# Optimization experiments

Measured on AMD Instinct MI355X. Metric: run time of the kernel, lower is better.

Reference implementation:

```python
import jax, jax.numpy as jnp
import numpy as np

N = 50000
E = 800000
IN_C = 128
HID = 64
HEADS = 4
NEG_SLOPE = 0.2
EPS = 1e-16


def setup_inputs() -> dict:
    key = jax.random.key(0)
    ks = jax.random.split(key, 12)
    x = jax.random.normal(ks[0], (N, IN_C), dtype=jnp.float32)
    edge_index = jax.random.randint(ks[1], (2, E), 0, N, dtype=jnp.int64)
    # layer 1: in -> (HEADS, HID), concat heads
    W1 = jax.random.normal(ks[2], (IN_C, HEADS * HID), dtype=jnp.float32) * (1.0 / np.sqrt(IN_C))
    a_src1 = jax.random.normal(ks[3], (HEADS, HID), dtype=jnp.float32) * 0.1
    a_dst1 = jax.random.normal(ks[4], (HEADS, HID), dtype=jnp.float32) * 0.1
    b1 = jnp.zeros((HEADS * HID,), dtype=jnp.float32)
    # layer 2: HEADS*HID -> (1, HID)
    W2 = jax.random.normal(ks[5], (HEADS * HID, HID), dtype=jnp.float32) * (1.0 / np.sqrt(HEADS * HID))
    a_src2 = jax.random.normal(ks[6], (1, HID), dtype=jnp.float32) * 0.1
    a_dst2 = jax.random.normal(ks[7], (1, HID), dtype=jnp.float32) * 0.1
    b2 = jnp.zeros((HID,), dtype=jnp.float32)
    return {"x": x, "edge_index": edge_index, "W1": W1, "a_src1": a_src1,
            "a_dst1": a_dst1, "b1": b1, "W2": W2, "a_src2": a_src2,
            "a_dst2": a_dst2, "b2": b2}


def _gat_conv(x, src, dst, W, a_src, a_dst, bias, heads, ch):
    n = x.shape[0]
    h = (x @ W).reshape(n, heads, ch)                       # [N,H,C]
    alpha_s = jnp.einsum('nhc,hc->nh', h, a_src)            # [N,H]
    alpha_d = jnp.einsum('nhc,hc->nh', h, a_dst)            # [N,H]
    e = jax.nn.leaky_relu(alpha_s[src] + alpha_d[dst], NEG_SLOPE)  # [E,H]
    # segment softmax over incoming edges of each dst node
    m = jax.ops.segment_max(e, dst, num_segments=n)         # [N,H]
    ex = jnp.exp(e - m[dst])
    denom = jax.ops.segment_sum(ex, dst, num_segments=n)    # [N,H]
    alpha = ex / (denom[dst] + EPS)                         # [E,H]
    msg = h[src] * alpha[:, :, None]                        # [E,H,C]
    out = jax.ops.segment_sum(msg, dst, num_segments=n)     # [N,H,C]
    return out.reshape(n, heads * ch) + bias


def reference(x, edge_index, W1, a_src1, a_dst1, b1, W2, a_src2, a_dst2, b2):
    src = edge_index[0]
    dst = edge_index[1]
    h = _gat_conv(x, src, dst, W1, a_src1, a_dst1, b1, HEADS, HID)
    h = jax.nn.elu(h)
    h = _gat_conv(h, src, dst, W2, a_src2, a_dst2, b2, 1, HID)
    h = jax.nn.elu(h)
    return h  # [N, HID] (output_dim == hidden_channels so no final linear)
```

## Files before the change

kernel.cpp:

```cpp
#include <hip/hip_runtime.h>
#include <math.h>

#define NN 50000
#define EE 800000
#define IN_C 128
#define HID 64
#define HEADS 4
#define SCAN_BLOCKS ((NN + 255) / 256)
#define EBLOCKS ((EE + 255) / 256)

typedef __attribute__((ext_vector_type(8))) short bf16x8;
typedef __attribute__((ext_vector_type(4))) float f32x4;

#if defined(__has_builtin)
#if __has_builtin(__builtin_amdgcn_fdot2_f32_bf16)
#define HAVE_FDOT2_BF16 1
#endif
#endif


__device__ inline unsigned short f2bf(float f) {
    unsigned u = __float_as_uint(f);
    return (unsigned short)((u + 0x7fff + ((u >> 16) & 1)) >> 16);
}
__device__ inline float bf2f(unsigned short s) {
    return __uint_as_float(((unsigned)s) << 16);
}
__device__ inline unsigned prm(unsigned a, unsigned b, unsigned sel) {
    return __builtin_amdgcn_perm(a, b, sel);
}
#ifdef HAVE_FDOT2_BF16
typedef __attribute__((ext_vector_type(2))) __bf16 bf2v;
__device__ inline float fdot2bf(unsigned h, unsigned w, float acc) {
    return __builtin_amdgcn_fdot2_f32_bf16(__builtin_bit_cast(bf2v, h),
                                           __builtin_bit_cast(bf2v, w), acc, false);
}
#else
__device__ inline float fdot2bf(unsigned h, unsigned w, float acc) {
    return acc + bf2f((unsigned short)(h & 0xffff)) * bf2f((unsigned short)(w & 0xffff))
               + bf2f((unsigned short)(h >> 16)) * bf2f((unsigned short)(w >> 16));
}
#endif

__device__ inline int wave_incl_scan(int v, int lane) {
    #pragma unroll
    for (int off = 1; off < 64; off <<= 1) {
        int t = __shfl_up(v, off);
        if (lane >= off) v += t;
    }
    return v;
}

__device__ inline int block256_excl_scan(int v, int tid, int* ws4) {
    int lane = tid & 63, wv = tid >> 6;
    int incl = wave_incl_scan(v, lane);
    if (lane == 63) ws4[wv] = incl;
    __syncthreads();
    if (tid == 0) {
        int run = 0;
        #pragma unroll
        for (int i = 0; i < 4; i++) { int t = ws4[i]; ws4[i] = run; run += t; }
    }
    __syncthreads();
    return incl + ws4[wv] - v;
}


__global__ void front_kernel(const int* __restrict__ ei, int* __restrict__ deg,
                             unsigned short* __restrict__ rank,
                             const float* __restrict__ W1, unsigned short* __restrict__ W1Thi,
                             unsigned short* __restrict__ W1Tlo,
                             const float* __restrict__ W2, unsigned short* __restrict__ W2Thi,
                             unsigned short* __restrict__ W2Tlo) {
    int b = blockIdx.x;
    int tid = threadIdx.x;
    if (b < EBLOCKS) {
        int i = b * 256 + tid;
        if (i < EE) rank[i] = (unsigned short)atomicAdd(&deg[ei[EE + i]], 1);
    } else if (b < EBLOCKS + 128) {
        int idx = (b - EBLOCKS) * 256 + tid;
        int r = idx >> 8, c = idx & 255;
        float v = W1[idx];
        unsigned short h = f2bf(v);
        W1Thi[c * 128 + r] = h;
        W1Tlo[c * 128 + r] = f2bf(v - bf2f(h));
    } else {
        int idx = (b - EBLOCKS - 128) * 256 + tid;
        int r = idx >> 6, c = idx & 63;
        float v = W2[idx];
        unsigned short h = f2bf(v);
        W2Thi[c * 256 + r] = h;
        W2Tlo[c * 256 + r] = f2bf(v - bf2f(h));
    }
}

__global__ void scan_fill_kernel(const int* __restrict__ deg,
                                 unsigned long long* __restrict__ desc,
                                 int* __restrict__ row_ptr) {
    __shared__ int ws4[4];
    __shared__ int sbase;
    int b = blockIdx.x, tid = threadIdx.x;
    int idx = b * 256 + tid;
    int d = (idx < NN) ? deg[idx] : 0;
    int excl = block256_excl_scan(d, tid, ws4);
    if (tid == 255) {
        unsigned total = (unsigned)(excl + d);
        __threadfence();
        atomicExch(&desc[b], (1ULL << 32) | (unsigned long long)total);
    }
    if (tid < 64) {
        int sum = 0;
        int hi = b;
        while (hi > 0) {
            int lo = hi - 64; if (lo < 0) lo = 0;
            int myi = lo + tid;
            unsigned v = 0;
            if (myi < hi) {
                unsigned long long d8;
                do { d8 = atomicAdd(&desc[myi], 0ULL); } while ((d8 >> 32) == 0);
                v = (unsigned)(d8 & 0xffffffffULL);
            }
            #pragma unroll
            for (int off = 32; off; off >>= 1) v += __shfl_down(v, off);
            v = __shfl(v, 0);
            sum += (int)v;
            hi = lo;
        }
        if (tid == 0) sbase = sum;
    }
    __syncthreads();
    int gbase = sbase;
    if (idx < NN) row_ptr[idx] = gbase + excl;
    if (b == gridDim.x - 1 && tid == 255) row_ptr[NN] = gbase + excl + d;
}

__global__ void scatter_kernel(const int* __restrict__ ei, const unsigned short* __restrict__ rank,
                               const int* __restrict__ row_ptr, unsigned short* __restrict__ csr_src) {
    int i = blockIdx.x * blockDim.x + threadIdx.x;
    if (i < EE) {
        int d = ei[EE + i];
        csr_src[row_ptr[d] + (int)rank[i]] = (unsigned short)ei[i];
    }
}

__global__ __launch_bounds__(256) void gemm1_mfma(
        const float* __restrict__ x,
        const unsigned short* __restrict__ Bhi, const unsigned short* __restrict__ Blo,
        const float* __restrict__ a_src, const float* __restrict__ a_dst,
        unsigned short* __restrict__ h1b, float* __restrict__ as1, float* __restrict__ ad1) {
    __shared__ unsigned short Ahi[64][136];
    __shared__ unsigned short Alo[64][136];
    int tid = threadIdx.x;
    int w = tid >> 6, lane = tid & 63;
    int lq = lane >> 4, lr = lane & 15;
    int brow = blockIdx.x * 64;
    {
        int row = tid >> 2;
        int col0 = (tid & 3) * 32;
        int gr = min(brow + row, NN - 1);
        #pragma unroll
        for (int i = 0; i < 32; i += 4) {
            float4 v = *(const float4*)(x + (size_t)gr * 128 + col0 + i);
            unsigned short h0 = f2bf(v.x), h1 = f2bf(v.y), h2 = f2bf(v.z), h3 = f2bf(v.w);
            Ahi[row][col0 + i + 0] = h0; Alo[row][col0 + i + 0] = f2bf(v.x - bf2f(h0));
            Ahi[row][col0 + i + 1] = h1; Alo[row][col0 + i + 1] = f2bf(v.y - bf2f(h1));
            Ahi[row][col0 + i + 2] = h2; Alo[row][col0 + i + 2] = f2bf(v.z - bf2f(h2));
            Ahi[row][col0 + i + 3] = h3; Alo[row][col0 + i + 3] = f2bf(v.w - bf2f(h3));
        }
    }
    __syncthreads();
    f32x4 acc[4][4];
    f32x4 zf = {0.f, 0.f, 0.f, 0.f};
    #pragma unroll
    for (int mi = 0; mi < 4; mi++)
        #pragma unroll
        for (int ni = 0; ni < 4; ni++) acc[mi][ni] = zf;
    #pragma unroll
    for (int q = 0; q < 4; q++) {
        int ko = q * 32 + lq * 8;
        bf16x8 ah[4], al[4];
        #pragma unroll
        for (int mi = 0; mi < 4; mi++) {
            ah[mi] = *(const bf16x8*)(const void*)&Ahi[mi * 16 + lr][ko];
            al[mi] = *(const bf16x8*)(const void*)&Alo[mi * 16 + lr][ko];
        }
        #pragma unroll
        for (int ni = 0; ni < 4; ni++) {
            size_t bo = (size_t)(w * 64 + ni * 16 + lr) * 128 + ko;
            bf16x8 bh = *(const bf16x8*)(const void*)(Bhi + bo);
            bf16x8 bl = *(const bf16x8*)(const void*)(Blo + bo);
            #pragma unroll
            for (int mi = 0; mi < 4; mi++) {
                acc[mi][ni] = __builtin_amdgcn_mfma_f32_16x16x32_bf16(al[mi], bh, acc[mi][ni], 0, 0, 0);
                acc[mi][ni] = __builtin_amdgcn_mfma_f32_16x16x32_bf16(ah[mi], bl, acc[mi][ni], 0, 0, 0);
                acc[mi][ni] = __builtin_amdgcn_mfma_f32_16x16x32_bf16(ah[mi], bh, acc[mi][ni], 0, 0, 0);
            }
        }
    }
    float asv[4], adv[4];
    #pragma unroll
    for (int ni = 0; ni < 4; ni++) {
        asv[ni] = a_src[w * 64 + ni * 16 + lr];
        adv[ni] = a_dst[w * 64 + ni * 16 + lr];
    }
    #pragma unroll
    for (int mi = 0; mi < 4; mi++) {
        f32x4 ps = zf, pd = zf;
        #pragma unroll
        for (int ni = 0; ni < 4; ni++)
            #pragma unroll
            for (int r = 0; r < 4; r++) {
                ps[r] += acc[mi][ni][r] * asv[ni];
                pd[r] += acc[mi][ni][r] * adv[ni];
            }
        #pragma unroll
        for (int m = 1; m < 16; m <<= 1)
            #pragma unroll
            for (int r = 0; r < 4; r++) {
                ps[r] += __shfl_xor(ps[r], m);
                pd[r] += __shfl_xor(pd[r], m);
            }
        #pragma unroll
        for (int r = 0; r < 4; r++) {
            int n = brow + mi * 16 + lq * 4 + r;
            if (lr == 0 && n < NN) { as1[n * 4 + w] = ps[r]; ad1[n * 4 + w] = pd[r]; }
        }
        #pragma unroll
        for (int ni = 0; ni < 4; ni++)
            #pragma unroll
            for (int r = 0; r < 4; r++) {
                int n = brow + mi * 16 + lq * 4 + r;
                if (n < NN)
                    h1b[(size_t)n * 256 + w * 64 + ni * 16 + lr] = f2bf(acc[mi][ni][r]);
            }
    }
}

__global__ __launch_bounds__(256) void gemm2_mfma(
        const unsigned short* __restrict__ Ab,
        const unsigned short* __restrict__ Bhi, const unsigned short* __restrict__ Blo,
        const float* __restrict__ a_src, const float* __restrict__ a_dst,
        unsigned short* __restrict__ g2b, float* __restrict__ as2, float* __restrict__ ad2) {
    int tid = threadIdx.x;
    int w = tid >> 6, lane = tid & 63;
    int lq = lane >> 4, lr = lane & 15;
    int wrow = blockIdx.x * 128 + w * 32;
    f32x4 acc[2][4];
    f32x4 zf = {0.f, 0.f, 0.f, 0.f};
    #pragma unroll
    for (int mi = 0; mi < 2; mi++)
        #pragma unroll
        for (int ni = 0; ni < 4; ni++) acc[mi][ni] = zf;
    int ra = min(wrow + lr, NN - 1);
    int rb = min(wrow + 16 + lr, NN - 1);
    #pragma unroll
    for (int q = 0; q < 8; q++) {
        int ko = q * 32 + lq * 8;
        bf16x8 ah0 = *(const bf16x8*)(const void*)(Ab + (size_t)ra * 256 + ko);
        bf16x8 ah1 = *(const bf16x8*)(const void*)(Ab + (size_t)rb * 256 + ko);
        #pragma unroll
        for (int ni = 0; ni < 4; ni++) {
            size_t bo = (size_t)(ni * 16 + lr) * 256 + ko;
            bf16x8 bh = *(const bf16x8*)(const void*)(Bhi + bo);
            bf16x8 bl = *(const bf16x8*)(const void*)(Blo + bo);
            acc[0][ni] = __builtin_amdgcn_mfma_f32_16x16x32_bf16(ah0, bl, acc[0][ni], 0, 0, 0);
            acc[0][ni] = __builtin_amdgcn_mfma_f32_16x16x32_bf16(ah0, bh, acc[0][ni], 0, 0, 0);
            acc[1][ni] = __builtin_amdgcn_mfma_f32_16x16x32_bf16(ah1, bl, acc[1][ni], 0, 0, 0);
            acc[1][ni] = __builtin_amdgcn_mfma_f32_16x16x32_bf16(ah1, bh, acc[1][ni], 0, 0, 0);
        }
    }
    float asv[4], adv[4];
    #pragma unroll
    for (int ni = 0; ni < 4; ni++) {
        asv[ni] = a_src[ni * 16 + lr];
        adv[ni] = a_dst[ni * 16 + lr];
    }
    #pragma unroll
    for (int mi = 0; mi < 2; mi++) {
        f32x4 ps = zf, pd = zf;
        #pragma unroll
        for (int ni = 0; ni < 4; ni++)
            #pragma unroll
            for (int r = 0; r < 4; r++) {
                ps[r] += acc[mi][ni][r] * asv[ni];
                pd[r] += acc[mi][ni][r] * adv[ni];
            }
        #pragma unroll
        for (int m = 1; m < 16; m <<= 1)
            #pragma unroll
            for (int r = 0; r < 4; r++) {
                ps[r] += __shfl_xor(ps[r], m);
                pd[r] += __shfl_xor(pd[r], m);
            }
        #pragma unroll
        for (int r = 0; r < 4; r++) {
            int n = wrow + mi * 16 + lq * 4 + r;
            if (lr == 0 && n < NN) { as2[n] = ps[r]; ad2[n] = pd[r]; }
        }
        #pragma unroll
        for (int ni = 0; ni < 4; ni++)
            #pragma unroll
            for (int r = 0; r < 4; r++) {
                int n = wrow + mi * 16 + lq * 4 + r;
                if (n < NN)
                    g2b[(size_t)n * 64 + ni * 16 + lr] = f2bf(acc[mi][ni][r]);
            }
    }
}

__global__ __launch_bounds__(256) void agg1_kernel(
        const unsigned short* __restrict__ h1b, const int* __restrict__ row_ptr,
        const unsigned short* __restrict__ csr_src, const float* __restrict__ as,
        const float* __restrict__ ad, const float* __restrict__ b1,
        unsigned short* __restrict__ h2b) {
    __shared__ int            ssrc[4][64];
    __shared__ unsigned short wbf[4][4][64];
    int tid = threadIdx.x;
    int wv = tid >> 6, lane = tid & 63;
    int n = blockIdx.x * 4 + wv;
    if (n >= NN) return;
    int start = row_ptr[n], end = row_ptr[n + 1];
    float4 adv = ((const float4*)ad)[n];
    int whead = lane >> 4;
    float4 acc = make_float4(0.f, 0.f, 0.f, 0.f);
    float d0 = 0.f, d1 = 0.f, d2 = 0.f, d3 = 0.f;
    for (int c0 = start; c0 < end; c0 += 64) {
        int m = min(64, end - c0);
        if (lane < m) {
            int s = (int)csr_src[c0 + lane];
            ssrc[wv][lane] = s;
            float4 asv = ((const float4*)as)[s];
            float e0 = asv.x + adv.x; e0 = e0 > 0.f ? e0 : 0.2f * e0; float x0 = __expf(e0);
            float e1 = asv.y + adv.y; e1 = e1 > 0.f ? e1 : 0.2f * e1; float x1 = __expf(e1);
            float e2 = asv.z + adv.z; e2 = e2 > 0.f ? e2 : 0.2f * e2; float x2 = __expf(e2);
            float e3 = asv.w + adv.w; e3 = e3 > 0.f ? e3 : 0.2f * e3; float x3 = __expf(e3);
            wbf[wv][0][lane] = f2bf(x0);
            wbf[wv][1][lane] = f2bf(x1);
            wbf[wv][2][lane] = f2bf(x2);
            wbf[wv][3][lane] = f2bf(x3);
            d0 += x0; d1 += x1; d2 += x2; d3 += x3;
        }
        int j = 0;
        for (; j + 8 <= m; j += 8) {
            int sj[8]; uint2 hj[8];
            #pragma unroll
            for (int u = 0; u < 8; u++) sj[u] = ssrc[wv][j + u];
            #pragma unroll
            for (int u = 0; u < 8; u++)
                hj[u] = ((const uint2*)h1b)[(size_t)sj[u] * 64 + lane];
            unsigned wp01 = *(const unsigned*)&wbf[wv][whead][j];
            unsigned wp23 = *(const unsigned*)&wbf[wv][whead][j + 2];
            unsigned wp45 = *(const unsigned*)&wbf[wv][whead][j + 4];
            unsigned wp67 = *(const unsigned*)&wbf[wv][whead][j + 6];
            acc.x = fdot2bf(prm(hj[1].x, hj[0].x, 0x05040100), wp01, acc.x);
            acc.y = fdot2bf(prm(hj[1].x, hj[0].x, 0x07060302), wp01, acc.y);
            acc.z = fdot2bf(prm(hj[1].y, hj[0].y, 0x05040100), wp01, acc.z);
            acc.w = fdot2bf(prm(hj[1].y, hj[0].y, 0x07060302), wp01, acc.w);
            acc.x = fdot2bf(prm(hj[3].x, hj[2].x, 0x05040100), wp23, acc.x);
            acc.y = fdot2bf(prm(hj[3].x, hj[2].x, 0x07060302), wp23, acc.y);
            acc.z = fdot2bf(prm(hj[3].y, hj[2].y, 0x05040100), wp23, acc.z);
            acc.w = fdot2bf(prm(hj[3].y, hj[2].y, 0x07060302), wp23, acc.w);
            acc.x = fdot2bf(prm(hj[5].x, hj[4].x, 0x05040100), wp45, acc.x);
            acc.y = fdot2bf(prm(hj[5].x, hj[4].x, 0x07060302), wp45, acc.y);
            acc.z = fdot2bf(prm(hj[5].y, hj[4].y, 0x05040100), wp45, acc.z);
            acc.w = fdot2bf(prm(hj[5].y, hj[4].y, 0x07060302), wp45, acc.w);
            acc.x = fdot2bf(prm(hj[7].x, hj[6].x, 0x05040100), wp67, acc.x);
            acc.y = fdot2bf(prm(hj[7].x, hj[6].x, 0x07060302), wp67, acc.y);
            acc.z = fdot2bf(prm(hj[7].y, hj[6].y, 0x05040100), wp67, acc.z);
            acc.w = fdot2bf(prm(hj[7].y, hj[6].y, 0x07060302), wp67, acc.w);
        }
        for (; j + 2 <= m; j += 2) {
            int s0 = ssrc[wv][j], s1 = ssrc[wv][j + 1];
            uint2 ha = ((const uint2*)h1b)[(size_t)s0 * 64 + lane];
            uint2 hb = ((const uint2*)h1b)[(size_t)s1 * 64 + lane];
            unsigned wp = *(const unsigned*)&wbf[wv][whead][j];
            acc.x = fdot2bf(prm(hb.x, ha.x, 0x05040100), wp, acc.x);
            acc.y = fdot2bf(prm(hb.x, ha.x, 0x07060302), wp, acc.y);
            acc.z = fdot2bf(prm(hb.y, ha.y, 0x05040100), wp, acc.z);
            acc.w = fdot2bf(prm(hb.y, ha.y, 0x07060302), wp, acc.w);
        }
        if (j < m) {
            int s = ssrc[wv][j];
            float w = bf2f(wbf[wv][whead][j]);
            ushort4 hv = ((const ushort4*)h1b)[(size_t)s * 64 + lane];
            acc.x += bf2f(hv.x) * w; acc.y += bf2f(hv.y) * w;
            acc.z += bf2f(hv.z) * w; acc.w += bf2f(hv.w) * w;
        }
    }
    #pragma unroll
    for (int off = 32; off; off >>= 1) {
        d0 += __shfl_down(d0, off); d1 += __shfl_down(d1, off);
        d2 += __shfl_down(d2, off); d3 += __shfl_down(d3, off);
    }
    d0 = __shfl(d0, 0); d1 = __shfl(d1, 0);
    d2 = __shfl(d2, 0); d3 = __shfl(d3, 0);
    float den = whead == 0 ? d0 : whead == 1 ? d1 : whead == 2 ? d2 : d3;
    float inv = 1.f / (den + 1e-16f);
    float4 bv = ((const float4*)b1)[lane];
    float4 r;
    r.x = acc.x * inv + bv.x; r.y = acc.y * inv + bv.y;
    r.z = acc.z * inv + bv.z; r.w = acc.w * inv + bv.w;
    r.x = r.x > 0.f ? r.x : expm1f(r.x);
    r.y = r.y > 0.f ? r.y : expm1f(r.y);
    r.z = r.z > 0.f ? r.z : expm1f(r.z);
    r.w = r.w > 0.f ? r.w : expm1f(r.w);
    ushort4 hv;
    hv.x = f2bf(r.x); hv.y = f2bf(r.y); hv.z = f2bf(r.z); hv.w = f2bf(r.w);
    ((ushort4*)h2b)[(size_t)n * 64 + lane] = hv;
}

__global__ __launch_bounds__(256) void agg2_kernel(
        const unsigned short* __restrict__ g2b, const int* __restrict__ row_ptr,
        const unsigned short* __restrict__ csr_src, const float* __restrict__ as,
        const float* __restrict__ ad, const float* __restrict__ b2,
        float* __restrict__ out) {
    __shared__ int            ssrc[4][64];
    __shared__ unsigned short wbf[4][64];
    int tid = threadIdx.x;
    int wv = tid >> 6, lane = tid & 63;
    int n = blockIdx.x * 4 + wv;
    if (n >= NN) return;
    int start = row_ptr[n], end = row_ptr[n + 1];
    float adv = ad[n];
    float acc = 0.f;
    float den = 0.f;
    for (int c0 = start; c0 < end; c0 += 64) {
        int m = min(64, end - c0);
        if (lane < m) {
            int s = (int)csr_src[c0 + lane];
            ssrc[wv][lane] = s;
            float e = as[s] + adv;
            e = e > 0.f ? e : 0.2f * e;
            float x = __expf(e);
            wbf[wv][lane] = f2bf(x);
            den += x;
        }
        int j = 0;
        for (; j + 8 <= m; j += 8) {
            int sj[8]; unsigned gj[8];
            #pragma unroll
            for (int u = 0; u < 8; u++) sj[u] = ssrc[wv][j + u];
            #pragma unroll
            for (int u = 0; u < 8; u++)
                gj[u] = g2b[(size_t)sj[u] * 64 + lane];
            unsigned wp01 = *(const unsigned*)&wbf[wv][j];
            unsigned wp23 = *(const unsigned*)&wbf[wv][j + 2];
            unsigned wp45 = *(const unsigned*)&wbf[wv][j + 4];
            unsigned wp67 = *(const unsigned*)&wbf[wv][j + 6];
            acc = fdot2bf(prm(gj[1], gj[0], 0x05040100), wp01, acc);
            acc = fdot2bf(prm(gj[3], gj[2], 0x05040100), wp23, acc);
            acc = fdot2bf(prm(gj[5], gj[4], 0x05040100), wp45, acc);
            acc = fdot2bf(prm(gj[7], gj[6], 0x05040100), wp67, acc);
        }
        for (; j + 2 <= m; j += 2) {
            int s0 = ssrc[wv][j], s1 = ssrc[wv][j + 1];
            unsigned g0 = g2b[(size_t)s0 * 64 + lane];
            unsigned g1 = g2b[(size_t)s1 * 64 + lane];
            unsigned wp = *(const unsigned*)&wbf[wv][j];
            acc = fdot2bf(prm(g1, g0, 0x05040100), wp, acc);
        }
        if (j < m) {
            int s = ssrc[wv][j];
            acc += bf2f(g2b[(size_t)s * 64 + lane]) * bf2f(wbf[wv][j]);
        }
    }
    #pragma unroll
    for (int off = 32; off; off >>= 1) den += __shfl_down(den, off);
    den = __shfl(den, 0);
    float inv = 1.f / (den + 1e-16f);
    float r = acc * inv + b2[lane];
    out[(size_t)n * 64 + lane] = r > 0.f ? r : expm1f(r);
}


extern "C" void kernel_launch(void* const* d_in, const int* in_sizes, int n_in,
                              void* d_out, int out_size, void* d_ws, size_t ws_size,
                              hipStream_t stream) {
    const float* x      = (const float*)d_in[0];
    const int*   ei     = (const int*)d_in[1];
    const float* W1     = (const float*)d_in[2];
    const float* a_src1 = (const float*)d_in[3];
    const float* a_dst1 = (const float*)d_in[4];
    const float* b1     = (const float*)d_in[5];
    const float* W2     = (const float*)d_in[6];
    const float* a_src2 = (const float*)d_in[7];
    const float* a_dst2 = (const float*)d_in[8];
    const float* b2     = (const float*)d_in[9];
    float* out = (float*)d_out;

    char* base = (char*)d_ws;
    size_t off = 0;
    auto alloc = [&](size_t bytes) -> void* {
        void* p = base + off;
        off = (off + bytes + 255) & ~(size_t)255;
        return p;
    };
    int*   deg     = (int*)alloc(NN * sizeof(int));
    unsigned long long* desc = (unsigned long long*)alloc(SCAN_BLOCKS * sizeof(unsigned long long));
    unsigned short* rank = (unsigned short*)alloc(EE * sizeof(unsigned short));
    int*   row_ptr = (int*)alloc((NN + 1) * sizeof(int));
    unsigned short* csr_src = (unsigned short*)alloc(EE * sizeof(unsigned short));
    unsigned short* W1Thi = (unsigned short*)alloc(256 * 128 * 2);
    unsigned short* W1Tlo = (unsigned short*)alloc(256 * 128 * 2);
    unsigned short* W2Thi = (unsigned short*)alloc(64 * 256 * 2);
    unsigned short* W2Tlo = (unsigned short*)alloc(64 * 256 * 2);
    unsigned short* h1b   = (unsigned short*)alloc((size_t)NN * 256 * 2);
    float* as1     = (float*)alloc((size_t)NN * 4 * sizeof(float));
    float* ad1     = (float*)alloc((size_t)NN * 4 * sizeof(float));
    unsigned short* h2b   = (unsigned short*)alloc((size_t)NN * 256 * 2);
    unsigned short* g2b   = (unsigned short*)alloc((size_t)NN * 64 * 2);
    float* as2     = (float*)alloc((size_t)NN * sizeof(float));
    float* ad2     = (float*)alloc((size_t)NN * sizeof(float));

    size_t clear_bytes = (size_t)((char*)(desc + SCAN_BLOCKS) - (char*)deg);
    hipMemsetAsync(deg, 0, clear_bytes, stream);

    front_kernel<<<EBLOCKS + 128 + 64, 256, 0, stream>>>(ei, deg, rank, W1, W1Thi, W1Tlo,
                                                         W2, W2Thi, W2Tlo);
    scan_fill_kernel<<<SCAN_BLOCKS, 256, 0, stream>>>(deg, desc, row_ptr);
    scatter_kernel<<<EBLOCKS, 256, 0, stream>>>(ei, rank, row_ptr, csr_src);

    gemm1_mfma<<<(NN + 63) / 64, 256, 0, stream>>>(x, W1Thi, W1Tlo,
                                                   a_src1, a_dst1, h1b, as1, ad1);
    agg1_kernel<<<(NN + 3) / 4, 256, 0, stream>>>(h1b, row_ptr, csr_src, as1, ad1, b1, h2b);
    gemm2_mfma<<<(NN + 127) / 128, 256, 0, stream>>>(h2b, W2Thi, W2Tlo,
                                                     a_src2, a_dst2, g2b, as2, ad2);
    agg2_kernel<<<(NN + 3) / 4, 256, 0, stream>>>(g2b, row_ptr, csr_src, as2, ad2, b2, out);
}
```

Baseline: 281.4 us.

## Precompute edge softmax weights in CSR order and pad rows to four

Edge attention weights (exp of leaky-relu logits) and per-node denominators are now computed once per edge in a scatter pass, which writes bf16 weights in CSR order and accumulates denominators with atomics. The separate scatter kernel is folded into that pass. Rows are padded to multiples of four with zero entries, so the aggregation kernels drop their remainder loops and process two edges per half-wave with a software-pipelined double-buffered gather of wider vectors. This moves exp work out of the latency-bound gather loops, at the cost of float atomics, extra memory traffic for the weight arrays, and an extra kernel per layer.

```diff
diff --git a/kernel.cpp b/kernel.cpp
--- a/kernel.cpp
+++ b/kernel.cpp
@@ -6,6 +6,7 @@
 #define IN_C 128
 #define HID 64
 #define HEADS 4
+#define EEP 950000
 #define SCAN_BLOCKS ((NN + 255) / 256)
 #define EBLOCKS ((EE + 255) / 256)
 
@@ -96,12 +97,16 @@
 
 __global__ void scan_fill_kernel(const int* __restrict__ deg,
                                  unsigned long long* __restrict__ desc,
-                                 int* __restrict__ row_ptr) {
+                                 int* __restrict__ row_ptr,
+                                 unsigned short* __restrict__ csr_src,
+                                 unsigned short* __restrict__ w1t,
+                                 unsigned short* __restrict__ w2t) {
     __shared__ int ws4[4];
     __shared__ int sbase;
     int b = blockIdx.x, tid = threadIdx.x;
     int idx = b * 256 + tid;
-    int d = (idx < NN) ? deg[idx] : 0;
+    int draw = (idx < NN) ? deg[idx] : 0;
+    int d = (draw + 3) & ~3;
     int excl = block256_excl_scan(d, tid, ws4);
     if (tid == 255) {
         unsigned total = (unsigned)(excl + d);
@@ -130,17 +135,16 @@
     }
     __syncthreads();
     int gbase = sbase;
-    if (idx < NN) row_ptr[idx] = gbase + excl;
+    if (idx < NN) {
+        int rp = gbase + excl;
+        row_ptr[idx] = rp;
+        for (int p = rp + draw; p < rp + d; ++p) {
+            csr_src[p] = 0;
+            w2t[p] = 0;
+            w1t[p] = 0; w1t[EEP + p] = 0; w1t[2 * EEP + p] = 0; w1t[3 * EEP + p] = 0;
+        }
+    }
     if (b == gridDim.x - 1 && tid == 255) row_ptr[NN] = gbase + excl + d;
-}
-
-__global__ void scatter_kernel(const int* __restrict__ ei, const unsigned short* __restrict__ rank,
-                               const int* __restrict__ row_ptr, unsigned short* __restrict__ csr_src) {
-    int i = blockIdx.x * blockDim.x + threadIdx.x;
-    if (i < EE) {
-        int d = ei[EE + i];
-        csr_src[row_ptr[d] + (int)rank[i]] = (unsigned short)ei[i];
-    }
 }
 
 __global__ __launch_bounds__(256) void gemm1_mfma(
@@ -308,168 +312,179 @@
     }
 }
 
-__global__ __launch_bounds__(256) void agg1_kernel(
+__global__ __launch_bounds__(256) void scatter_w1_kernel(
+        const int* __restrict__ ei, const unsigned short* __restrict__ rank,
+        const int* __restrict__ row_ptr, const float* __restrict__ as1,
+        const float* __restrict__ ad1, unsigned short* __restrict__ csr_src,
+        unsigned short* __restrict__ w1t, float* __restrict__ den1) {
+    int i = blockIdx.x * 256 + threadIdx.x;
+    if (i >= EE) return;
+    int s = ei[i], d = ei[EE + i];
+    int pos = row_ptr[d] + (int)rank[i];
+    csr_src[pos] = (unsigned short)s;
+    float4 av = ((const float4*)as1)[s];
+    float4 bv = ((const float4*)ad1)[d];
+    float e0 = av.x + bv.x; e0 = e0 > 0.f ? e0 : 0.2f * e0; float x0 = __expf(e0);
+    float e1 = av.y + bv.y; e1 = e1 > 0.f ? e1 : 0.2f * e1; float x1 = __expf(e1);
+    float e2 = av.z + bv.z; e2 = e2 > 0.f ? e2 : 0.2f * e2; float x2 = __expf(e2);
+    float e3 = av.w + bv.w; e3 = e3 > 0.f ? e3 : 0.2f * e3; float x3 = __expf(e3);
+    w1t[pos]           = f2bf(x0);
+    w1t[EEP + pos]     = f2bf(x1);
+    w1t[2 * EEP + pos] = f2bf(x2);
+    w1t[3 * EEP + pos] = f2bf(x3);
+    atomicAdd(den1 + d * 4 + 0, x0);
+    atomicAdd(den1 + d * 4 + 1, x1);
+    atomicAdd(den1 + d * 4 + 2, x2);
+    atomicAdd(den1 + d * 4 + 3, x3);
+}
+
+__global__ __launch_bounds__(256) void w2_kernel(
+        const int* __restrict__ ei, const unsigned short* __restrict__ rank,
+        const int* __restrict__ row_ptr, const float* __restrict__ as2,
+        const float* __restrict__ ad2, unsigned short* __restrict__ w2t,
+        float* __restrict__ den2) {
+    int i = blockIdx.x * 256 + threadIdx.x;
+    if (i >= EE) return;
+    int s = ei[i], d = ei[EE + i];
+    int pos = row_ptr[d] + (int)rank[i];
+    float e = as2[s] + ad2[d];
+    e = e > 0.f ? e : 0.2f * e;
+    float x = __expf(e);
+    w2t[pos] = f2bf(x);
+    atomicAdd(den2 + d, x);
+}
+
+__global__ __launch_bounds__(256, 4) void agg1_kernel(
         const unsigned short* __restrict__ h1b, const int* __restrict__ row_ptr,
-        const unsigned short* __restrict__ csr_src, const float* __restrict__ as,
-        const float* __restrict__ ad, const float* __restrict__ b1,
+        const unsigned short* __restrict__ csr_src, const unsigned short* __restrict__ w1t,
+        const float* __restrict__ den1, const float* __restrict__ b1,
         unsigned short* __restrict__ h2b) {
-    __shared__ int            ssrc[4][64];
-    __shared__ unsigned short wbf[4][4][64];
+    __shared__ unsigned ssrc32[4][32];
     int tid = threadIdx.x;
     int wv = tid >> 6, lane = tid & 63;
     int n = blockIdx.x * 4 + wv;
     if (n >= NN) return;
     int start = row_ptr[n], end = row_ptr[n + 1];
-    float4 adv = ((const float4*)ad)[n];
-    int whead = lane >> 4;
-    float4 acc = make_float4(0.f, 0.f, 0.f, 0.f);
-    float d0 = 0.f, d1 = 0.f, d2 = 0.f, d3 = 0.f;
+    int H = lane >> 5, l5 = lane & 31;
+    int h = l5 >> 3;
+    const unsigned short* __restrict__ wr = w1t + (size_t)h * EEP;
+    const unsigned short* __restrict__ hp = h1b + l5 * 8;
+    f32x4 a0 = {0.f, 0.f, 0.f, 0.f}, a1 = {0.f, 0.f, 0.f, 0.f};
+    uint4 LA0, LB0, LA1, LB1;
+    unsigned wp0, wp1;
     for (int c0 = start; c0 < end; c0 += 64) {
         int m = min(64, end - c0);
-        if (lane < m) {
-            int s = (int)csr_src[c0 + lane];
-            ssrc[wv][lane] = s;
-            float4 asv = ((const float4*)as)[s];
-            float e0 = asv.x + adv.x; e0 = e0 > 0.f ? e0 : 0.2f * e0; float x0 = __expf(e0);
-            float e1 = asv.y + adv.y; e1 = e1 > 0.f ? e1 : 0.2f * e1; float x1 = __expf(e1);
-            float e2 = asv.z + adv.z; e2 = e2 > 0.f ? e2 : 0.2f * e2; float x2 = __expf(e2);
-            float e3 = asv.w + adv.w; e3 = e3 > 0.f ? e3 : 0.2f * e3; float x3 = __expf(e3);
-            wbf[wv][0][lane] = f2bf(x0);
-            wbf[wv][1][lane] = f2bf(x1);
-            wbf[wv][2][lane] = f2bf(x2);
-            wbf[wv][3][lane] = f2bf(x3);
-            d0 += x0; d1 += x1; d2 += x2; d3 += x3;
-        }
-        int j = 0;
-        for (; j + 8 <= m; j += 8) {
-            int sj[8]; uint2 hj[8];
-            #pragma unroll
-            for (int u = 0; u < 8; u++) sj[u] = ssrc[wv][j + u];
-            #pragma unroll
-            for (int u = 0; u < 8; u++)
-                hj[u] = ((const uint2*)h1b)[(size_t)sj[u] * 64 + lane];
-            unsigned wp01 = *(const unsigned*)&wbf[wv][whead][j];
-            unsigned wp23 = *(const unsigned*)&wbf[wv][whead][j + 2];
-            unsigned wp45 = *(const unsigned*)&wbf[wv][whead][j + 4];
-            unsigned wp67 = *(const unsigned*)&wbf[wv][whead][j + 6];
-            acc.x = fdot2bf(prm(hj[1].x, hj[0].x, 0x05040100), wp01, acc.x);
-            acc.y = fdot2bf(prm(hj[1].x, hj[0].x, 0x07060302), wp01, acc.y);
-            acc.z = fdot2bf(prm(hj[1].y, hj[0].y, 0x05040100), wp01, acc.z);
-            acc.w = fdot2bf(prm(hj[1].y, hj[0].y, 0x07060302), wp01, acc.w);
-            acc.x = fdot2bf(prm(hj[3].x, hj[2].x, 0x05040100), wp23, acc.x);
-            acc.y = fdot2bf(prm(hj[3].x, hj[2].x, 0x07060302), wp23, acc.y);
-            acc.z = fdot2bf(prm(hj[3].y, hj[2].y, 0x05040100), wp23, acc.z);
-            acc.w = fdot2bf(prm(hj[3].y, hj[2].y, 0x07060302), wp23, acc.w);
-            acc.x = fdot2bf(prm(hj[5].x, hj[4].x, 0x05040100), wp45, acc.x);
-            acc.y = fdot2bf(prm(hj[5].x, hj[4].x, 0x07060302), wp45, acc.y);
-            acc.z = fdot2bf(prm(hj[5].y, hj[4].y, 0x05040100), wp45, acc.z);
-            acc.w = fdot2bf(prm(hj[5].y, hj[4].y, 0x07060302), wp45, acc.w);
-            acc.x = fdot2bf(prm(hj[7].x, hj[6].x, 0x05040100), wp67, acc.x);
-            acc.y = fdot2bf(prm(hj[7].x, hj[6].x, 0x07060302), wp67, acc.y);
-            acc.z = fdot2bf(prm(hj[7].y, hj[6].y, 0x05040100), wp67, acc.z);
-            acc.w = fdot2bf(prm(hj[7].y, hj[6].y, 0x07060302), wp67, acc.w);
-        }
-        for (; j + 2 <= m; j += 2) {
-            int s0 = ssrc[wv][j], s1 = ssrc[wv][j + 1];
-            uint2 ha = ((const uint2*)h1b)[(size_t)s0 * 64 + lane];
-            uint2 hb = ((const uint2*)h1b)[(size_t)s1 * 64 + lane];
-            unsigned wp = *(const unsigned*)&wbf[wv][whead][j];
-            acc.x = fdot2bf(prm(hb.x, ha.x, 0x05040100), wp, acc.x);
-            acc.y = fdot2bf(prm(hb.x, ha.x, 0x07060302), wp, acc.y);
-            acc.z = fdot2bf(prm(hb.y, ha.y, 0x05040100), wp, acc.z);
-            acc.w = fdot2bf(prm(hb.y, ha.y, 0x07060302), wp, acc.w);
-        }
-        if (j < m) {
-            int s = ssrc[wv][j];
-            float w = bf2f(wbf[wv][whead][j]);
-            ushort4 hv = ((const ushort4*)h1b)[(size_t)s * 64 + lane];
-            acc.x += bf2f(hv.x) * w; acc.y += bf2f(hv.y) * w;
-            acc.z += bf2f(hv.z) * w; acc.w += bf2f(hv.w) * w;
-        }
-    }
-    #pragma unroll
-    for (int off = 32; off; off >>= 1) {
-        d0 += __shfl_down(d0, off); d1 += __shfl_down(d1, off);
-        d2 += __shfl_down(d2, off); d3 += __shfl_down(d3, off);
-    }
-    d0 = __shfl(d0, 0); d1 = __shfl(d1, 0);
-    d2 = __shfl(d2, 0); d3 = __shfl(d3, 0);
-    float den = whead == 0 ? d0 : whead == 1 ? d1 : whead == 2 ? d2 : d3;
-    float inv = 1.f / (den + 1e-16f);
-    float4 bv = ((const float4*)b1)[lane];
-    float4 r;
-    r.x = acc.x * inv + bv.x; r.y = acc.y * inv + bv.y;
-    r.z = acc.z * inv + bv.z; r.w = acc.w * inv + bv.w;
-    r.x = r.x > 0.f ? r.x : expm1f(r.x);
-    r.y = r.y > 0.f ? r.y : expm1f(r.y);
-    r.z = r.z > 0.f ? r.z : expm1f(r.z);
-    r.w = r.w > 0.f ? r.w : expm1f(r.w);
-    ushort4 hv;
-    hv.x = f2bf(r.x); hv.y = f2bf(r.y); hv.z = f2bf(r.z); hv.w = f2bf(r.w);
-    ((ushort4*)h2b)[(size_t)n * 64 + lane] = hv;
-}
-
-__global__ __launch_bounds__(256) void agg2_kernel(
+        if (lane < (m >> 1))
+            ssrc32[wv][lane] = *(const unsigned*)(const void*)(csr_src + c0 + 2 * lane);
+        int G = m >> 2;
+        auto LD = [&](int g, uint4& A, uint4& B, unsigned& wp) {
+            unsigned both = ssrc32[wv][2 * g + H];
+            int ia = (int)(both & 0xffffu), ib = (int)(both >> 16);
+            A = *(const uint4*)(const void*)(hp + ia * 256);
+            B = *(const uint4*)(const void*)(hp + ib * 256);
+            wp = *(const unsigned*)(const void*)(wr + c0 + 4 * g + 2 * H);
+        };
+        auto CMP = [&](const uint4& A, const uint4& B, unsigned wp) {
+            a0.x = fdot2bf(prm(B.x, A.x, 0x05040100), wp, a0.x);
+            a0.y = fdot2bf(prm(B.x, A.x, 0x07060302), wp, a0.y);
+            a0.z = fdot2bf(prm(B.y, A.y, 0x05040100), wp, a0.z);
+            a0.w = fdot2bf(prm(B.y, A.y, 0x07060302), wp, a0.w);
+            a1.x = fdot2bf(prm(B.z, A.z, 0x05040100), wp, a1.x);
+            a1.y = fdot2bf(prm(B.z, A.z, 0x07060302), wp, a1.y);
+            a1.z = fdot2bf(prm(B.w, A.w, 0x05040100), wp, a1.z);
+            a1.w = fdot2bf(prm(B.w, A.w, 0x07060302), wp, a1.w);
+        };
+        LD(0, LA0, LB0, wp0);
+        if (G > 1) LD(1, LA1, LB1, wp1);
+        int g = 0;
+        while (true) {
+            CMP(LA0, LB0, wp0);
+            if (g + 2 < G) LD(g + 2, LA0, LB0, wp0);
+            if (++g >= G) break;
+            CMP(LA1, LB1, wp1);
+            if (g + 2 < G) LD(g + 2, LA1, LB1, wp1);
+            if (++g >= G) break;
+        }
+    }
+    a0.x += __shfl_xor(a0.x, 32); a0.y += __shfl_xor(a0.y, 32);
+    a0.z += __shfl_xor(a0.z, 32); a0.w += __shfl_xor(a0.w, 32);
+    a1.x += __shfl_xor(a1.x, 32); a1.y += __shfl_xor(a1.y, 32);
+    a1.z += __shfl_xor(a1.z, 32); a1.w += __shfl_xor(a1.w, 32);
+    if (H == 0) {
+        float inv = 1.f / (den1[n * 4 + h] + 1e-16f);
+        float4 bb0 = *(const float4*)(b1 + l5 * 8);
+        float4 bb1 = *(const float4*)(b1 + l5 * 8 + 4);
+        float r0 = a0.x * inv + bb0.x, r1 = a0.y * inv + bb0.y;
+        float r2 = a0.z * inv + bb0.z, r3 = a0.w * inv + bb0.w;
+        float r4 = a1.x * inv + bb1.x, r5 = a1.y * inv + bb1.y;
+        float r6 = a1.z * inv + bb1.z, r7 = a1.w * inv + bb1.w;
+        r0 = r0 > 0.f ? r0 : expm1f(r0); r1 = r1 > 0.f ? r1 : expm1f(r1);
+        r2 = r2 > 0.f ? r2 : expm1f(r2); r3 = r3 > 0.f ? r3 : expm1f(r3);
+        r4 = r4 > 0.f ? r4 : expm1f(r4); r5 = r5 > 0.f ? r5 : expm1f(r5);
+        r6 = r6 > 0.f ? r6 : expm1f(r6); r7 = r7 > 0.f ? r7 : expm1f(r7);
+        uint4 st;
+        st.x = (unsigned)f2bf(r0) | ((unsigned)f2bf(r1) << 16);
+        st.y = (unsigned)f2bf(r2) | ((unsigned)f2bf(r3) << 16);
+        st.z = (unsigned)f2bf(r4) | ((unsigned)f2bf(r5) << 16);
+        st.w = (unsigned)f2bf(r6) | ((unsigned)f2bf(r7) << 16);
+        *(uint4*)(void*)(h2b + (size_t)n * 256 + l5 * 8) = st;
+    }
+}
+
+__global__ __launch_bounds__(256, 4) void agg2_kernel(
         const unsigned short* __restrict__ g2b, const int* __restrict__ row_ptr,
-        const unsigned short* __restrict__ csr_src, const float* __restrict__ as,
-        const float* __restrict__ ad, const float* __restrict__ b2,
+        const unsigned short* __restrict__ csr_src, const unsigned short* __restrict__ w2t,
+        const float* __restrict__ den2, const float* __restrict__ b2,
         float* __restrict__ out) {
-    __shared__ int            ssrc[4][64];
-    __shared__ unsigned short wbf[4][64];
+    __shared__ unsigned ssrc32[4][32];
     int tid = threadIdx.x;
     int wv = tid >> 6, lane = tid & 63;
     int n = blockIdx.x * 4 + wv;
     if (n >= NN) return;
     int start = row_ptr[n], end = row_ptr[n + 1];
-    float adv = ad[n];
-    float acc = 0.f;
-    float den = 0.f;
+    int H = lane >> 5, l5 = lane & 31;
+    const unsigned short* __restrict__ gp = g2b + l5 * 2;
+    float ax = 0.f, ay = 0.f;
+    unsigned A0, B0, w0, A1, B1, w1v;
     for (int c0 = start; c0 < end; c0 += 64) {
         int m = min(64, end - c0);
-        if (lane < m) {
-            int s = (int)csr_src[c0 + lane];
-            ssrc[wv][lane] = s;
-            float e = as[s] + adv;
-            e = e > 0.f ? e : 0.2f * e;
-            float x = __expf(e);
-            wbf[wv][lane] = f2bf(x);
-            den += x;
-        }
-        int j = 0;
-        for (; j + 8 <= m; j += 8) {
-            int sj[8]; unsigned gj[8];
-            #pragma unroll
-            for (int u = 0; u < 8; u++) sj[u] = ssrc[wv][j + u];
-            #pragma unroll
-            for (int u = 0; u < 8; u++)
-                gj[u] = g2b[(size_t)sj[u] * 64 + lane];
-            unsigned wp01 = *(const unsigned*)&wbf[wv][j];
-            unsigned wp23 = *(const unsigned*)&wbf[wv][j + 2];
-            unsigned wp45 = *(const unsigned*)&wbf[wv][j + 4];
-            unsigned wp67 = *(const unsigned*)&wbf[wv][j + 6];
-            acc = fdot2bf(prm(gj[1], gj[0], 0x05040100), wp01, acc);
-            acc = fdot2bf(prm(gj[3], gj[2], 0x05040100), wp23, acc);
-            acc = fdot2bf(prm(gj[5], gj[4], 0x05040100), wp45, acc);
-            acc = fdot2bf(prm(gj[7], gj[6], 0x05040100), wp67, acc);
-        }
-        for (; j + 2 <= m; j += 2) {
-            int s0 = ssrc[wv][j], s1 = ssrc[wv][j + 1];
-            unsigned g0 = g2b[(size_t)s0 * 64 + lane];
-            unsigned g1 = g2b[(size_t)s1 * 64 + lane];
-            unsigned wp = *(const unsigned*)&wbf[wv][j];
-            acc = fdot2bf(prm(g1, g0, 0x05040100), wp, acc);
-        }
-        if (j < m) {
-            int s = ssrc[wv][j];
-            acc += bf2f(g2b[(size_t)s * 64 + lane]) * bf2f(wbf[wv][j]);
-        }
-    }
-    #pragma unroll
-    for (int off = 32; off; off >>= 1) den += __shfl_down(den, off);
-    den = __shfl(den, 0);
-    float inv = 1.f / (den + 1e-16f);
-    float r = acc * inv + b2[lane];
-    out[(size_t)n * 64 + lane] = r > 0.f ? r : expm1f(r);
+        if (lane < (m >> 1))
+            ssrc32[wv][lane] = *(const unsigned*)(const void*)(csr_src + c0 + 2 * lane);
+        int G = m >> 2;
+        auto LD = [&](int g, unsigned& A, unsigned& B, unsigned& wp) {
+            unsigned both = ssrc32[wv][2 * g + H];
+            int ia = (int)(both & 0xffffu), ib = (int)(both >> 16);
+            A = *(const unsigned*)(const void*)(gp + ia * 64);
+            B = *(const unsigned*)(const void*)(gp + ib * 64);
+            wp = *(const unsigned*)(const void*)(w2t + c0 + 4 * g + 2 * H);
+        };
+        auto CMP = [&](unsigned A, unsigned B, unsigned wp) {
+            ax = fdot2bf(prm(B, A, 0x05040100), wp, ax);
+            ay = fdot2bf(prm(B, A, 0x07060302), wp, ay);
+        };
+        LD(0, A0, B0, w0);
+        if (G > 1) LD(1, A1, B1, w1v);
+        int g = 0;
+        while (true) {
+            CMP(A0, B0, w0);
+            if (g + 2 < G) LD(g + 2, A0, B0, w0);
+            if (++g >= G) break;
+            CMP(A1, B1, w1v);
+            if (g + 2 < G) LD(g + 2, A1, B1, w1v);
+            if (++g >= G) break;
+        }
+    }
+    ax += __shfl_xor(ax, 32);
+    ay += __shfl_xor(ay, 32);
+    if (H == 0) {
+        float inv = 1.f / (den2[n] + 1e-16f);
+        float2 bv = ((const float2*)b2)[l5];
+        float rx = ax * inv + bv.x;
+        float ry = ay * inv + bv.y;
+        rx = rx > 0.f ? rx : expm1f(rx);
+        ry = ry > 0.f ? ry : expm1f(ry);
+        *(float2*)(out + (size_t)n * 64 + l5 * 2) = make_float2(rx, ry);
+    }
 }
 
 
@@ -497,9 +512,13 @@
     };
     int*   deg     = (int*)alloc(NN * sizeof(int));
     unsigned long long* desc = (unsigned long long*)alloc(SCAN_BLOCKS * sizeof(unsigned long long));
+    float* den1    = (float*)alloc((size_t)NN * 4 * sizeof(float));
+    float* den2    = (float*)alloc((size_t)NN * sizeof(float));
     unsigned short* rank = (unsigned short*)alloc(EE * sizeof(unsigned short));
     int*   row_ptr = (int*)alloc((NN + 1) * sizeof(int));
-    unsigned short* csr_src = (unsigned short*)alloc(EE * sizeof(unsigned short));
+    unsigned short* csr_src = (unsigned short*)alloc((size_t)EEP * sizeof(unsigned short));
+    unsigned short* w1t = (unsigned short*)alloc((size_t)4 * EEP * sizeof(unsigned short));
+    unsigned short* w2t = (unsigned short*)alloc((size_t)EEP * sizeof(unsigned short));
     unsigned short* W1Thi = (unsigned short*)alloc(256 * 128 * 2);
     unsigned short* W1Tlo = (unsigned short*)alloc(256 * 128 * 2);
     unsigned short* W2Thi = (unsigned short*)alloc(64 * 256 * 2);
@@ -508,22 +527,24 @@
     float* as1     = (float*)alloc((size_t)NN * 4 * sizeof(float));
     float* ad1     = (float*)alloc((size_t)NN * 4 * sizeof(float));
     unsigned short* h2b   = (unsigned short*)alloc((size_t)NN * 256 * 2);
-    unsigned short* g2b   = (unsigned short*)alloc((size_t)NN * 64 * 2);
-    float* as2     = (float*)alloc((size_t)NN * sizeof(float));
-    float* ad2     = (float*)alloc((size_t)NN * sizeof(float));
-
-    size_t clear_bytes = (size_t)((char*)(desc + SCAN_BLOCKS) - (char*)deg);
+    unsigned short* g2b = h1b;
+    float* as2 = as1;
+    float* ad2 = ad1;
+
+    size_t clear_bytes = (size_t)((char*)(den2 + NN) - (char*)deg);
     hipMemsetAsync(deg, 0, clear_bytes, stream);
 
     front_kernel<<<EBLOCKS + 128 + 64, 256, 0, stream>>>(ei, deg, rank, W1, W1Thi, W1Tlo,
                                                          W2, W2Thi, W2Tlo);
-    scan_fill_kernel<<<SCAN_BLOCKS, 256, 0, stream>>>(deg, desc, row_ptr);
-    scatter_kernel<<<EBLOCKS, 256, 0, stream>>>(ei, rank, row_ptr, csr_src);
+    scan_fill_kernel<<<SCAN_BLOCKS, 256, 0, stream>>>(deg, desc, row_ptr, csr_src, w1t, w2t);
 
     gemm1_mfma<<<(NN + 63) / 64, 256, 0, stream>>>(x, W1Thi, W1Tlo,
                                                    a_src1, a_dst1, h1b, as1, ad1);
-    agg1_kernel<<<(NN + 3) / 4, 256, 0, stream>>>(h1b, row_ptr, csr_src, as1, ad1, b1, h2b);
+    scatter_w1_kernel<<<EBLOCKS, 256, 0, stream>>>(ei, rank, row_ptr, as1, ad1,
+                                                   csr_src, w1t, den1);
+    agg1_kernel<<<(NN + 3) / 4, 256, 0, stream>>>(h1b, row_ptr, csr_src, w1t, den1, b1, h2b);
     gemm2_mfma<<<(NN + 127) / 128, 256, 0, stream>>>(h2b, W2Thi, W2Tlo,
                                                      a_src2, a_dst2, g2b, as2, ad2);
-    agg2_kernel<<<(NN + 3) / 4, 256, 0, stream>>>(g2b, row_ptr, csr_src, as2, ad2, b2, out);
-}
+    w2_kernel<<<EBLOCKS, 256, 0, stream>>>(ei, rank, row_ptr, as2, ad2, w2t, den2);
+    agg2_kernel<<<(NN + 3) / 4, 256, 0, stream>>>(g2b, row_ptr, csr_src, w2t, den2, b2, out);
+}
```

Result: slower. 490.3 us (+74.3%).
